# Kernel optimization log

Measured on AMD Instinct MI355X. Metric: run time of the kernel, lower is better.

The kernel has to match this reference:

```python
import jax, jax.numpy as jnp
import numpy as np

CUTOFF = 0.5          # radius_graph cutoff r
MAX_NEIGHBORS = 32    # max_num_neighbors
NUM_GRAPHS = 8192     # B molecules
ATOMS = 64            # M atoms per molecule (equal-size graphs)


def setup_inputs() -> dict:
    key = jax.random.key(0)
    n = NUM_GRAPHS * ATOMS
    pos = jax.random.uniform(key, (n, 3), dtype=jnp.float32)  # atoms in unit cube
    batch = jnp.arange(n, dtype=jnp.int32) // ATOMS           # graph id per atom
    return {"pos": pos, "batch": batch}


def _radius_graph(pos):
    """Fixed-shape radius_graph: per node, up to K nearest in-radius neighbors
    within the same graph (equal-size graphs of ATOMS nodes, matching `batch`
    from setup_inputs). Invalid (out-of-radius / padded) edges are self-loops
    flagged False in `valid`."""
    M, K, r = ATOMS, MAX_NEIGHBORS, CUTOFF
    N = pos.shape[0]
    B = N // M
    p = pos.reshape(B, M, 3)
    # pairwise squared distances per graph via gram trick: (B, M, M)
    n2 = jnp.sum(p * p, axis=-1)
    g = jnp.einsum('bmd,bnd->bmn', p, p)
    sq = jnp.maximum(n2[:, :, None] + n2[:, None, :] - 2.0 * g, 0.0)
    # exclude self-loops (radius_graph default loop=False)
    sq = jnp.where(jnp.eye(M, dtype=bool)[None], jnp.inf, sq)
    neg_sq, nbr = jax.lax.top_k(-sq, K)            # K nearest per node: (B, M, K)
    valid = (-neg_sq) <= r * r                     # within cutoff
    base = (jnp.arange(B, dtype=jnp.int32) * M)[:, None, None]
    tgt = base + jnp.arange(M, dtype=jnp.int32)[None, :, None]  # target node i
    src = base + nbr.astype(jnp.int32)                           # source neighbor j
    src = jnp.where(valid, src, jnp.broadcast_to(tgt, src.shape))  # pad -> self
    row = src.reshape(-1)                                        # edge source
    col = jnp.broadcast_to(tgt, src.shape).reshape(-1)           # edge target
    edge_index = jnp.stack([row, col])             # (2, N*K), source_to_target
    return edge_index, valid.reshape(-1)


def reference(pos, batch):
    edge_index, valid = _radius_graph(pos)
    row, col = edge_index
    diff = pos[row] - pos[col]                     # gathered pairwise vectors
    sq = jnp.sum(diff * diff, axis=-1)
    # safe norm: padded self-loop edges have sq == 0 -> weight 0, grad-safe
    edge_weight = jnp.where(valid, jnp.sqrt(jnp.where(valid, sq, 1.0)), 0.0)
    return edge_index, edge_weight, valid
```

## Files before the change

### kernel.cpp

```cpp
#include <hip/hip_runtime.h>
#include <math.h>

#define GRAPHS 8192
#define M 64
#define KNBR 32
#define NK (GRAPHS * M * KNBR)


template <int J>
__device__ __forceinline__ unsigned lane_xor(unsigned x) {
  if constexpr (J == 1) {
    return (unsigned)__builtin_amdgcn_update_dpp((int)x, (int)x, 0xB1, 0xF, 0xF, false);
  } else if constexpr (J == 2) {
    return (unsigned)__builtin_amdgcn_update_dpp((int)x, (int)x, 0x4E, 0xF, 0xF, false);
  } else if constexpr (J == 4) {
    int t = __builtin_amdgcn_update_dpp((int)x, (int)x, 0x141, 0xF, 0xF, false);
    return (unsigned)__builtin_amdgcn_update_dpp(t, t, 0x1B, 0xF, 0xF, false);
  } else if constexpr (J == 8) {
    return (unsigned)__builtin_amdgcn_update_dpp((int)x, (int)x, 0x128, 0xF, 0xF, false);
  } else {
    return (unsigned)__shfl_xor((int)x, J, 64);
  }
}

__global__ __launch_bounds__(256) void radius_graph_kernel(
    const float* __restrict__ pos, float* __restrict__ out) {
#pragma clang fp contract(off)
  __shared__ float sx[M], sy[M], sz[M], sn2[M];

  const int g    = blockIdx.x;
  const int tid  = threadIdx.x;
  const int lane = tid & 63;
  const int wave = tid >> 6;
  const int base = g * M;

  if (tid < M) {
    float x = pos[(size_t)(base + tid) * 3 + 0];
    float y = pos[(size_t)(base + tid) * 3 + 1];
    float z = pos[(size_t)(base + tid) * 3 + 2];
    sx[tid] = x; sy[tid] = y; sz[tid] = z;
    sn2[tid] = (x * x + y * y) + z * z;
  }
  __syncthreads();

  const float xj = sx[lane], yj = sy[lane], zj = sz[lane], n2j = sn2[lane];

  for (int tq = 0; tq < 4; ++tq) {
    const int i0 = wave * 16 + tq * 4;

    unsigned key[4];
    #pragma unroll
    for (int c = 0; c < 4; ++c) {
      const int i = i0 + c;
      const float xi = sx[i], yi = sy[i], zi = sz[i], n2i = sn2[i];
      float gd = __builtin_fmaf(zi, zj, __builtin_fmaf(yi, yj, xi * xj));
      float sq = fmaxf((n2i + n2j) - 2.0f * gd, 0.0f);
      unsigned kb = __float_as_uint(sq);
      key[c] = (lane == i) ? (0x7FFFFFC0u | (unsigned)lane)
                           : ((kb & 0xFFFFFFC0u) | (unsigned)lane);
    }

#define CMPX(KK, J)                                                     \
    {                                                                   \
      const bool dir = (((lane & (KK)) == 0) == ((lane & (J)) == 0));   \
      _Pragma("unroll")                                                 \
      for (int c = 0; c < 4; ++c) {                                     \
        unsigned o = lane_xor<J>(key[c]);                               \
        bool lt = key[c] < o;                                           \
        key[c] = (lt == dir) ? key[c] : o;                              \
      }                                                                 \
    }
    CMPX(2, 1)
    CMPX(4, 2)  CMPX(4, 1)
    CMPX(8, 4)  CMPX(8, 2)  CMPX(8, 1)
    CMPX(16, 8) CMPX(16, 4) CMPX(16, 2) CMPX(16, 1)
    CMPX(32, 16) CMPX(32, 8) CMPX(32, 4) CMPX(32, 2) CMPX(32, 1)
    CMPX(64, 32) CMPX(64, 16) CMPX(64, 8) CMPX(64, 4) CMPX(64, 2) CMPX(64, 1)
#undef CMPX

    #pragma unroll
    for (int p = 0; p < 2; ++p) {
      unsigned kA = key[2 * p], kB = key[2 * p + 1];
      unsigned kBsw = (unsigned)__shfl_xor((int)kB, 32, 64);
      unsigned k = (lane < 32) ? kA : kBsw;

      const int i = i0 + 2 * p + (lane >> 5);
      const int nb = (int)(k & 63u);

      const float xi = sx[i],  yi = sy[i],  zi = sz[i],  n2i = sn2[i];
      const float xn = sx[nb], yn = sy[nb], zn = sz[nb], n2n = sn2[nb];

      float gde = __builtin_fmaf(zi, zn, __builtin_fmaf(yi, yn, xi * xn));
      float sqe = fmaxf((n2i + n2n) - 2.0f * gde, 0.0f);
      bool valid = (sqe <= 0.25f);

      int tgt = base + i;
      int src = valid ? (base + nb) : tgt;

      float dx = xn - xi, dy = yn - yi, dz = zn - zi;
      float w  = valid ? sqrtf((dx * dx + dy * dy) + dz * dz) : 0.0f;

      size_t e = (size_t)tgt * KNBR + (size_t)(lane & 31);
      __builtin_nontemporal_store((float)src, &out[e]);
      __builtin_nontemporal_store((float)tgt, &out[(size_t)NK + e]);
      __builtin_nontemporal_store(w,          &out[2 * (size_t)NK + e]);
      __builtin_nontemporal_store(valid ? 1.0f : 0.0f, &out[3 * (size_t)NK + e]);
    }
  }
}

extern "C" void kernel_launch(void* const* d_in, const int* in_sizes, int n_in,
                              void* d_out, int out_size, void* d_ws, size_t ws_size,
                              hipStream_t stream) {
  const float* pos = (const float*)d_in[0];
  float* out = (float*)d_out;
  radius_graph_kernel<<<GRAPHS, 256, 0, stream>>>(pos, out);
}
```

Before: 300.7 us.

## Replace full bitonic sort with ballot compaction when in-radius count fits K

```diff
diff --git a/kernel.cpp b/kernel.cpp
--- a/kernel.cpp
+++ b/kernel.cpp
@@ -6,6 +6,15 @@
 #define KNBR 32
 #define NK (GRAPHS * M * KNBR)
 
+
+__device__ __forceinline__ float readlane_f(float v, int l) {
+  return __int_as_float(__builtin_amdgcn_readlane(__float_as_int(v), l));
+}
+
+__device__ __forceinline__ int mbcnt64(unsigned long long m) {
+  return (int)__builtin_amdgcn_mbcnt_hi((unsigned)(m >> 32),
+           __builtin_amdgcn_mbcnt_lo((unsigned)m, 0u));
+}
 
 template <int J>
 __device__ __forceinline__ unsigned lane_xor(unsigned x) {
@@ -26,85 +35,75 @@
 __global__ __launch_bounds__(256) void radius_graph_kernel(
     const float* __restrict__ pos, float* __restrict__ out) {
 #pragma clang fp contract(off)
-  __shared__ float sx[M], sy[M], sz[M], sn2[M];
-
   const int g    = blockIdx.x;
   const int tid  = threadIdx.x;
   const int lane = tid & 63;
   const int wave = tid >> 6;
   const int base = g * M;
 
-  if (tid < M) {
-    float x = pos[(size_t)(base + tid) * 3 + 0];
-    float y = pos[(size_t)(base + tid) * 3 + 1];
-    float z = pos[(size_t)(base + tid) * 3 + 2];
-    sx[tid] = x; sy[tid] = y; sz[tid] = z;
-    sn2[tid] = (x * x + y * y) + z * z;
-  }
-  __syncthreads();
+  const float xj = pos[(size_t)(base + lane) * 3 + 0];
+  const float yj = pos[(size_t)(base + lane) * 3 + 1];
+  const float zj = pos[(size_t)(base + lane) * 3 + 2];
+  const float n2j = (xj * xj + yj * yj) + zj * zj;
 
-  const float xj = sx[lane], yj = sy[lane], zj = sz[lane], n2j = sn2[lane];
+  for (int t = 0; t < 16; ++t) {
+    const int i = wave * 16 + t;
+    const float xi  = readlane_f(xj, i);
+    const float yi  = readlane_f(yj, i);
+    const float zi  = readlane_f(zj, i);
+    const float n2i = readlane_f(n2j, i);
 
-  for (int tq = 0; tq < 4; ++tq) {
-    const int i0 = wave * 16 + tq * 4;
+    float gd = __builtin_fmaf(zi, zj, __builtin_fmaf(yi, yj, xi * xj));
+    float sq = fmaxf((n2i + n2j) - 2.0f * gd, 0.0f);
 
-    unsigned key[4];
-    #pragma unroll
-    for (int c = 0; c < 4; ++c) {
-      const int i = i0 + c;
-      const float xi = sx[i], yi = sy[i], zi = sz[i], n2i = sn2[i];
-      float gd = __builtin_fmaf(zi, zj, __builtin_fmaf(yi, yj, xi * xj));
-      float sq = fmaxf((n2i + n2j) - 2.0f * gd, 0.0f);
+    const bool inr = (sq <= 0.25f) & (lane != i);
+    const unsigned long long m = __ballot(inr);
+    const int T = __popcll(m);
+    const int tgt = base + i;
+
+    if (T <= KNBR) {
+      int slot = inr ? mbcnt64(m) : (T + mbcnt64(~m));
+      if (slot < KNBR) {
+        float w    = inr ? __builtin_amdgcn_sqrtf(sq) : 0.0f;
+        float srcf = inr ? (float)(base + lane) : (float)tgt;
+        size_t e = (size_t)tgt * KNBR + (size_t)slot;
+        __builtin_nontemporal_store(srcf,        &out[e]);
+        __builtin_nontemporal_store((float)tgt,  &out[(size_t)NK + e]);
+        __builtin_nontemporal_store(w,           &out[2 * (size_t)NK + e]);
+        __builtin_nontemporal_store(inr ? 1.0f : 0.0f, &out[3 * (size_t)NK + e]);
+      }
+    } else {
       unsigned kb = __float_as_uint(sq);
-      key[c] = (lane == i) ? (0x7FFFFFC0u | (unsigned)lane)
-                           : ((kb & 0xFFFFFFC0u) | (unsigned)lane);
-    }
+      unsigned key = inr ? ((kb & 0xFFFFFFC0u) | (unsigned)lane)
+                         : (0x7FFFFFC0u | (unsigned)lane);
 
 #define CMPX(KK, J)                                                     \
-    {                                                                   \
-      const bool dir = (((lane & (KK)) == 0) == ((lane & (J)) == 0));   \
-      _Pragma("unroll")                                                 \
-      for (int c = 0; c < 4; ++c) {                                     \
-        unsigned o = lane_xor<J>(key[c]);                               \
-        bool lt = key[c] < o;                                           \
-        key[c] = (lt == dir) ? key[c] : o;                              \
-      }                                                                 \
-    }
-    CMPX(2, 1)
-    CMPX(4, 2)  CMPX(4, 1)
-    CMPX(8, 4)  CMPX(8, 2)  CMPX(8, 1)
-    CMPX(16, 8) CMPX(16, 4) CMPX(16, 2) CMPX(16, 1)
-    CMPX(32, 16) CMPX(32, 8) CMPX(32, 4) CMPX(32, 2) CMPX(32, 1)
-    CMPX(64, 32) CMPX(64, 16) CMPX(64, 8) CMPX(64, 4) CMPX(64, 2) CMPX(64, 1)
+      {                                                                 \
+        const bool dir = (((lane & (KK)) == 0) == ((lane & (J)) == 0)); \
+        unsigned o = lane_xor<J>(key);                                  \
+        bool lt = key < o;                                              \
+        key = (lt == dir) ? key : o;                                    \
+      }
+      CMPX(2, 1)
+      CMPX(4, 2)   CMPX(4, 1)
+      CMPX(8, 4)   CMPX(8, 2)  CMPX(8, 1)
+      CMPX(16, 8)  CMPX(16, 4) CMPX(16, 2) CMPX(16, 1)
+      CMPX(32, 16) CMPX(32, 8) CMPX(32, 4) CMPX(32, 2) CMPX(32, 1)
 #undef CMPX
+      unsigned o32 = (unsigned)__shfl_xor((int)key, 32, 64);
+      unsigned mn  = key < o32 ? key : o32;
 
-    #pragma unroll
-    for (int p = 0; p < 2; ++p) {
-      unsigned kA = key[2 * p], kB = key[2 * p + 1];
-      unsigned kBsw = (unsigned)__shfl_xor((int)kB, 32, 64);
-      unsigned k = (lane < 32) ? kA : kBsw;
-
-      const int i = i0 + 2 * p + (lane >> 5);
-      const int nb = (int)(k & 63u);
-
-      const float xi = sx[i],  yi = sy[i],  zi = sz[i],  n2i = sn2[i];
-      const float xn = sx[nb], yn = sy[nb], zn = sz[nb], n2n = sn2[nb];
-
-      float gde = __builtin_fmaf(zi, zn, __builtin_fmaf(yi, yn, xi * xn));
-      float sqe = fmaxf((n2i + n2n) - 2.0f * gde, 0.0f);
-      bool valid = (sqe <= 0.25f);
-
-      int tgt = base + i;
-      int src = valid ? (base + nb) : tgt;
-
-      float dx = xn - xi, dy = yn - yi, dz = zn - zi;
-      float w  = valid ? sqrtf((dx * dx + dy * dy) + dz * dz) : 0.0f;
-
-      size_t e = (size_t)tgt * KNBR + (size_t)(lane & 31);
-      __builtin_nontemporal_store((float)src, &out[e]);
-      __builtin_nontemporal_store((float)tgt, &out[(size_t)NK + e]);
-      __builtin_nontemporal_store(w,          &out[2 * (size_t)NK + e]);
-      __builtin_nontemporal_store(valid ? 1.0f : 0.0f, &out[3 * (size_t)NK + e]);
+      if (lane < KNBR) {
+        float sq_t = __uint_as_float(mn & 0xFFFFFFC0u);
+        bool valid = (sq_t <= 0.25f);
+        float w    = valid ? __builtin_amdgcn_sqrtf(sq_t) : 0.0f;
+        int   src  = valid ? (base + (int)(mn & 63u)) : tgt;
+        size_t e = (size_t)tgt * KNBR + (size_t)lane;
+        __builtin_nontemporal_store((float)src, &out[e]);
+        __builtin_nontemporal_store((float)tgt, &out[(size_t)NK + e]);
+        __builtin_nontemporal_store(w,          &out[2 * (size_t)NK + e]);
+        __builtin_nontemporal_store(valid ? 1.0f : 0.0f, &out[3 * (size_t)NK + e]);
+      }
     }
   }
 }
```

Result: faster. 274.4 us (-8.7%).
